# Optimization experiments

Hardware: AMD Instinct MI355X
Metric: run time of the kernel (lower is better)

## Reference

```python
import jax, jax.numpy as jnp
import numpy as np

D_MODEL = 1024
N_HEADS = 16
HEAD_DIM = D_MODEL // N_HEADS


def setup_inputs() -> dict:
    key = jax.random.key(0)
    ks = jax.random.split(key, 5)
    T, B = 2048, 2
    x = jax.random.normal(ks[0], (T, B, D_MODEL), dtype=jnp.float32)
    s = 1.0 / np.sqrt(D_MODEL)
    Wq = jax.random.normal(ks[1], (D_MODEL, D_MODEL), dtype=jnp.float32) * s
    Wk = jax.random.normal(ks[2], (D_MODEL, D_MODEL), dtype=jnp.float32) * s
    Wv = jax.random.normal(ks[3], (D_MODEL, D_MODEL), dtype=jnp.float32) * s
    Wo = jax.random.normal(ks[4], (D_MODEL, D_MODEL), dtype=jnp.float32) * s
    return {"x": x, "Wq": Wq, "Wk": Wk, "Wv": Wv, "Wo": Wo}


def reference(x, Wq, Wk, Wv, Wo):
    T, B, C = x.shape
    H, D = N_HEADS, HEAD_DIM

    def split_heads(t):
        # (T,B,C) -> (B,H,T,D), matching view+permute(1,2,0,3)
        return t.reshape(T, B, H, D).transpose(1, 2, 0, 3)

    q = split_heads(x @ Wq.T)
    k = split_heads(x @ Wk.T)
    v = split_heads(x @ Wv.T)

    scale = 1.0 / jnp.sqrt(jnp.asarray(D, dtype=x.dtype))
    scores = jnp.einsum('bhqd,bhkd->bhqk', q, k) * scale  # (B,H,T,T)
    causal = jnp.tril(jnp.ones((T, T), dtype=bool))
    scores = jnp.where(causal, scores, jnp.asarray(-jnp.inf, dtype=scores.dtype))
    probs = jax.nn.softmax(scores, axis=-1)
    ctx = jnp.einsum('bhqk,bhkd->bhqd', probs, v)  # (B,H,T,D)
    ctx = ctx.transpose(2, 0, 1, 3).reshape(T, B, C)
    return ctx @ Wo.T
```

## Files before the change

### kernel.cpp

```cpp
#include <hip/hip_runtime.h>
#include <hip/hip_bf16.h>

#define TT 2048
#define BB 2
#define CC 1024
#define HH 16
#define DD 64
#define MM (TT * BB)

typedef short bf16x8 __attribute__((ext_vector_type(8)));
typedef float f32x4  __attribute__((ext_vector_type(4)));

__device__ inline ushort f2b(float f) {
    union { float f; unsigned u; } v; v.f = f;
    unsigned r = v.u + 0x7FFFu + ((v.u >> 16) & 1u);
    return (ushort)(r >> 16);
}

__device__ inline unsigned pack_bf16(float a, float b) {
    __hip_bfloat162 h = __float22bfloat162_rn(make_float2(a, b));
    union { __hip_bfloat162 h; unsigned u; } c; c.h = h;
    return c.u;
}

__device__ inline void gload_lds16(const ushort* g, ushort* l) {
    __builtin_amdgcn_global_load_lds(
        (const __attribute__((address_space(1))) void*)g,
        (__attribute__((address_space(3))) void*)l, 16, 0, 0);
}

#define XQUADS (MM * CC / 4)
#define WQUADS (CC * CC / 4)
__global__ __launch_bounds__(256) void conv_all(const float* __restrict__ x,
                                                const float* __restrict__ Wq,
                                                const float* __restrict__ Wk,
                                                const float* __restrict__ Wv,
                                                const float* __restrict__ Wo,
                                                ushort* __restrict__ dst) {
    int idx = blockIdx.x * 256 + threadIdx.x;
    const float* src;
    int off;
    if (idx < XQUADS) {
        src = x; off = idx;
    } else {
        int wi = (idx - XQUADS) >> 18;
        off = (idx - XQUADS) & (WQUADS - 1);
        src = (wi == 0) ? Wq : (wi == 1) ? Wk : (wi == 2) ? Wv : Wo;
    }
    float4 v = ((const float4*)src)[off];
    ushort4 o = {f2b(v.x), f2b(v.y), f2b(v.z), f2b(v.w)};
    ((ushort4*)dst)[idx] = o;
}

__global__ __launch_bounds__(256) void gemm_qkv(const ushort* __restrict__ A,
                                                const ushort* __restrict__ B0,
                                                const ushort* __restrict__ B1,
                                                const ushort* __restrict__ B2,
                                                ushort* __restrict__ Oq,
                                                ushort* __restrict__ Ok,
                                                ushort* __restrict__ Ov) {
    __shared__ __align__(16) ushort As[128 * 32];
    __shared__ __align__(16) ushort Bs[128 * 32];

    const int tid = threadIdx.x;
    const int wave = tid >> 6, lane = tid & 63;
    const int quad = lane >> 4, l16 = lane & 15;
    const int wm = wave >> 1, wn = wave & 1;

    const int bm = blockIdx.x * 128;
    const int by = blockIdx.y;
    const int wsel = by >> 3;
    const ushort* Bp = (wsel == 0) ? B0 : (wsel == 1) ? B1 : B2;
    const int bn = (by & 7) * 128;

    const int srow = lane >> 2;
    const int scol = (lane & 3) * 8;

    f32x4 acc[4][4];
#pragma unroll
    for (int i = 0; i < 4; i++)
#pragma unroll
        for (int j = 0; j < 4; j++) acc[i][j] = (f32x4){0.f, 0.f, 0.f, 0.f};

    for (int k0 = 0; k0 < CC; k0 += 32) {
#pragma unroll
        for (int i = 0; i < 2; i++) {
            const int rbase = wave * 32 + i * 16;
            gload_lds16(A + (size_t)(bm + rbase + srow) * CC + k0 + scol,
                        As + rbase * 32);
            gload_lds16(Bp + (size_t)(bn + rbase + srow) * CC + k0 + scol,
                        Bs + rbase * 32);
        }
        __syncthreads();

        bf16x8 af[4], bf[4];
#pragma unroll
        for (int mi = 0; mi < 4; mi++)
            af[mi] = *(const bf16x8*)(As + (wm * 64 + mi * 16 + l16) * 32 + quad * 8);
#pragma unroll
        for (int ni = 0; ni < 4; ni++)
            bf[ni] = *(const bf16x8*)(Bs + (wn * 64 + ni * 16 + l16) * 32 + quad * 8);
#pragma unroll
        for (int mi = 0; mi < 4; mi++)
#pragma unroll
            for (int ni = 0; ni < 4; ni++)
                acc[mi][ni] = __builtin_amdgcn_mfma_f32_16x16x32_bf16(
                    af[mi], bf[ni], acc[mi][ni], 0, 0, 0);
        __syncthreads();
    }

#pragma unroll
    for (int mi = 0; mi < 4; mi++) {
#pragma unroll
        for (int r = 0; r < 4; r++) {
            const int m = bm + wm * 64 + mi * 16 + quad * 4 + r;
#pragma unroll
            for (int ni = 0; ni < 4; ni++) {
                const int colg = bn + wn * 64 + ni * 16 + l16;
                float v = acc[mi][ni][r];
                if (wsel == 0) v *= 0.18033688f;
                const int t = m >> 1, b = m & 1;
                const int h = colg >> 6, d = colg & 63;
                ushort* dst = (wsel == 0) ? Oq : (wsel == 1) ? Ok : Ov;
                dst[(((size_t)(b * HH + h)) * TT + t) * DD + d] = f2b(v);
            }
        }
    }
}

__global__ __launch_bounds__(256) void gemm_out(const ushort* __restrict__ A,
                                                const ushort* __restrict__ Bm,
                                                float* __restrict__ Of) {
    __shared__ __align__(16) ushort As[128 * 32];
    __shared__ __align__(16) ushort Bs[64 * 32];

    const int tid = threadIdx.x;
    const int wave = tid >> 6, lane = tid & 63;
    const int quad = lane >> 4, l16 = lane & 15;

    const int bm = blockIdx.x * 128;
    const int bn = blockIdx.y * 64;

    const int srow = lane >> 2;
    const int scol = (lane & 3) * 8;

    f32x4 acc[2][4];
#pragma unroll
    for (int i = 0; i < 2; i++)
#pragma unroll
        for (int j = 0; j < 4; j++) acc[i][j] = (f32x4){0.f, 0.f, 0.f, 0.f};

    for (int k0 = 0; k0 < CC; k0 += 32) {
#pragma unroll
        for (int i = 0; i < 2; i++) {
            const int rbase = wave * 32 + i * 16;
            gload_lds16(A + (size_t)(bm + rbase + srow) * CC + k0 + scol,
                        As + rbase * 32);
        }
        gload_lds16(Bm + (size_t)(bn + wave * 16 + srow) * CC + k0 + scol,
                    Bs + wave * 16 * 32);
        __syncthreads();

        bf16x8 af[2], bf[4];
#pragma unroll
        for (int mi = 0; mi < 2; mi++)
            af[mi] = *(const bf16x8*)(As + (wave * 32 + mi * 16 + l16) * 32 + quad * 8);
#pragma unroll
        for (int ni = 0; ni < 4; ni++)
            bf[ni] = *(const bf16x8*)(Bs + (ni * 16 + l16) * 32 + quad * 8);
#pragma unroll
        for (int mi = 0; mi < 2; mi++)
#pragma unroll
            for (int ni = 0; ni < 4; ni++)
                acc[mi][ni] = __builtin_amdgcn_mfma_f32_16x16x32_bf16(
                    af[mi], bf[ni], acc[mi][ni], 0, 0, 0);
        __syncthreads();
    }

#pragma unroll
    for (int mi = 0; mi < 2; mi++)
#pragma unroll
        for (int r = 0; r < 4; r++) {
            const int m = bm + wave * 32 + mi * 16 + quad * 4 + r;
#pragma unroll
            for (int ni = 0; ni < 4; ni++)
                Of[(size_t)m * CC + bn + ni * 16 + l16] = acc[mi][ni][r];
        }
}

__global__ __launch_bounds__(256) void prep_kv(const ushort* __restrict__ Kb,
                                               const ushort* __restrict__ Vb,
                                               ushort* __restrict__ Kf,
                                               ushort* __restrict__ Vf) {
    __shared__ __align__(16) ushort Ls[64 * 72];
    const int tile = blockIdx.x;
    const int bh   = blockIdx.y;
    const int t    = threadIdx.x;
    const size_t src = (size_t)bh * TT * DD + (size_t)tile * 64 * DD;
    const size_t dst = (size_t)bh * TT * DD + (size_t)tile * 4096;

#pragma unroll
    for (int i = 0; i < 2; i++) {
        int e = t + i * 256;
        int r = e >> 3, kc = (e & 7) * 8;
        *(uint4*)(Ls + r * 72 + kc) = *(const uint4*)(Kb + src + r * 64 + kc);
    }
    __syncthreads();
#pragma unroll
    for (int i = 0; i < 2; i++) {
        int o = t + i * 256;
        int c = o >> 8, nb = (o >> 6) & 3, lane = o & 63;
        int quad = lane >> 4, l16 = lane & 15;
        int j = nb * 16 + l16, k0 = c * 32 + quad * 8;
        *(uint4*)(Kf + dst + (size_t)o * 8) = *(const uint4*)(Ls + j * 72 + k0);
    }
    __syncthreads();

#pragma unroll
    for (int i = 0; i < 2; i++) {
        int e = t + i * 256;
        int r = e >> 3, kc = (e & 7) * 8;
        *(uint4*)(Ls + r * 72 + kc) = *(const uint4*)(Vb + src + r * 64 + kc);
    }
    __syncthreads();
#pragma unroll
    for (int i = 0; i < 2; i++) {
        int o = t + i * 256;
        int c = o >> 8, db = (o >> 6) & 3, lane = o & 63;
        int quad = lane >> 4, l16 = lane & 15;
        int d = db * 16 + l16;
        ushort tmp[8];
#pragma unroll
        for (int u = 0; u < 8; u++) {
            int j = 16 * ((8 * c + u) >> 2) + 4 * quad + (u & 3);
            tmp[u] = Ls[j * 72 + d];
        }
        *(uint4*)(Vf + dst + (size_t)o * 8) = *(uint4*)tmp;
    }
}

template <bool DIAG>
__device__ __forceinline__ void attn_step64(const bf16x8* qa,
                                            f32x4* O,
                                            float* l,
                                            const bf16x8* kf, const bf16x8* vf,
                                            int j0, int qg0, int quad) {
#pragma unroll
    for (int m = 0; m < 2; m++) {
        f32x4 S[4];
#pragma unroll
        for (int nb = 0; nb < 4; nb++) S[nb] = (f32x4){0.f, 0.f, 0.f, 0.f};
#pragma unroll
        for (int c = 0; c < 2; c++)
#pragma unroll
            for (int nb = 0; nb < 4; nb++)
                S[nb] = __builtin_amdgcn_mfma_f32_16x16x32_bf16(
                    kf[c * 4 + nb], qa[m * 2 + c], S[nb], 0, 0, 0);

        const int qg = qg0 + m * 16;
        float p[4][4];
#pragma unroll
        for (int nb = 0; nb < 4; nb++)
#pragma unroll
            for (int r = 0; r < 4; r++) {
                float s = S[nb][r];
                if (DIAG) { if (j0 + nb * 16 + quad * 4 + r > qg) s = -1e30f; }
                p[nb][r] = __builtin_amdgcn_exp2f(s);
            }
#pragma unroll
        for (int nb = 0; nb < 4; nb++)
            l[m] += (p[nb][0] + p[nb][1]) + (p[nb][2] + p[nb][3]);

        union { unsigned w[4]; bf16x8 v; } pa0, pa1;
#pragma unroll
        for (int w = 0; w < 4; w++) {
            const int nb = w >> 1;
            const int rb = (w & 1) * 2;
            pa0.w[w] = pack_bf16(p[nb][rb], p[nb][rb + 1]);
            pa1.w[w] = pack_bf16(p[2 + nb][rb], p[2 + nb][rb + 1]);
        }
#pragma unroll
        for (int db = 0; db < 4; db++)
            O[m * 4 + db] = __builtin_amdgcn_mfma_f32_16x16x32_bf16(
                pa0.v, vf[db], O[m * 4 + db], 0, 0, 0);
#pragma unroll
        for (int db = 0; db < 4; db++)
            O[m * 4 + db] = __builtin_amdgcn_mfma_f32_16x16x32_bf16(
                pa1.v, vf[4 + db], O[m * 4 + db], 0, 0, 0);
    }
}

__global__ __launch_bounds__(256, 1) void attn_mfma(const ushort* __restrict__ Qb,
                                                    const ushort* __restrict__ Kf,
                                                    const ushort* __restrict__ Vf,
                                                    ushort* __restrict__ ctx) {
    __shared__ __align__(16) ushort KV[2][8192];

    const int tid  = threadIdx.x;
    const int wave = tid >> 6;
    const int lane = tid & 63;
    const int quad = lane >> 4;
    const int l16  = lane & 15;

    const int bidx = blockIdx.x;
    const int xcd  = bidx & 7;
    const int slot = bidx >> 3;
    const int bh   = xcd * 4 + (slot >> 3);
    const int p    = slot & 7;

    const int qtA = p, qtB = 15 - p;
    const int q0A = qtA * 128 + wave * 32;
    const int q0B = qtB * 128 + wave * 32;
    const int qgA = q0A + l16;
    const int qgB = q0B + l16;

    const size_t baseQK = (size_t)bh * TT * DD;

    bf16x8 qaA[4], qaB[4];
#pragma unroll
    for (int m = 0; m < 2; m++) {
        const ushort* qp = Qb + baseQK + (size_t)(q0A + m * 16 + l16) * DD + quad * 8;
        qaA[m * 2 + 0] = *(const bf16x8*)(qp);
        qaA[m * 2 + 1] = *(const bf16x8*)(qp + 32);
        const ushort* qp2 = Qb + baseQK + (size_t)(q0B + m * 16 + l16) * DD + quad * 8;
        qaB[m * 2 + 0] = *(const bf16x8*)(qp2);
        qaB[m * 2 + 1] = *(const bf16x8*)(qp2 + 32);
    }

    f32x4 OA[8], OB[8];
#pragma unroll
    for (int i = 0; i < 8; i++) {
        OA[i] = (f32x4){0.f, 0.f, 0.f, 0.f};
        OB[i] = (f32x4){0.f, 0.f, 0.f, 0.f};
    }
    float lA[2] = {0.f, 0.f}, lB[2] = {0.f, 0.f};

    const int dA = 2 * qtA + (wave >> 1);
    const int dB = 2 * qtB + (wave >> 1);
    const int ktmax = 2 * qtB + 1;

    const ushort* Kfp = Kf + baseQK;
    const ushort* Vfp = Vf + baseQK;

    auto stage = [&](int buf, const ushort* kp, const ushort* vp) {
#pragma unroll
        for (int i = 0; i < 2; i++) {
            const int ch = wave * 2 + i;
            gload_lds16(kp + (ch << 9) + lane * 8, &KV[buf][ch << 9]);
            gload_lds16(vp + (ch << 9) + lane * 8, &KV[buf][(8 + ch) << 9]);
        }
    };

    stage(0, Kfp, Vfp);
    __syncthreads();

    int cur = 0;
    for (int kt = 0; kt <= ktmax; kt++) {
        if (kt < ktmax) stage(cur ^ 1, Kfp + 4096, Vfp + 4096);

        bf16x8 kf[8], vf[8];
#pragma unroll
        for (int i = 0; i < 8; i++) {
            kf[i] = *(const bf16x8*)(&KV[cur][i << 9] + lane * 8);
            vf[i] = *(const bf16x8*)(&KV[cur][(8 + i) << 9] + lane * 8);
        }

        const int j0 = kt * 64;
        if (kt < dB)
            attn_step64<false>(qaB, OB, lB, kf, vf, j0, qgB, quad);
        else if (kt == dB)
            attn_step64<true >(qaB, OB, lB, kf, vf, j0, qgB, quad);

        if (kt < dA)
            attn_step64<false>(qaA, OA, lA, kf, vf, j0, qgA, quad);
        else if (kt == dA)
            attn_step64<true >(qaA, OA, lA, kf, vf, j0, qgA, quad);

        __syncthreads();
        cur ^= 1;
        Kfp += 4096;
        Vfp += 4096;
    }

#pragma unroll
    for (int m = 0; m < 2; m++) {
        lA[m] += __shfl_xor(lA[m], 16); lA[m] += __shfl_xor(lA[m], 32);
        lB[m] += __shfl_xor(lB[m], 16); lB[m] += __shfl_xor(lB[m], 32);
    }

    const int b = bh >> 4, h = bh & 15;
#pragma unroll
    for (int m = 0; m < 2; m++)
#pragma unroll
        for (int r = 0; r < 4; r++) {
            const float invA = 1.f / __shfl(lA[m], quad * 4 + r);
            const float invB = 1.f / __shfl(lB[m], quad * 4 + r);
            const int tA = q0A + m * 16 + quad * 4 + r;
            const int tB = q0B + m * 16 + quad * 4 + r;
#pragma unroll
            for (int db = 0; db < 4; db++) {
                ctx[((size_t)tA * BB + b) * CC + h * DD + db * 16 + l16] =
                    f2b(OA[m * 4 + db][r] * invA);
                ctx[((size_t)tB * BB + b) * CC + h * DD + db * 16 + l16] =
                    f2b(OB[m * 4 + db][r] * invB);
            }
        }
}

extern "C" void kernel_launch(void* const* d_in, const int* in_sizes, int n_in,
                              void* d_out, int out_size, void* d_ws, size_t ws_size,
                              hipStream_t stream) {
    const float* x  = (const float*)d_in[0];
    const float* Wq = (const float*)d_in[1];
    const float* Wk = (const float*)d_in[2];
    const float* Wv = (const float*)d_in[3];
    const float* Wo = (const float*)d_in[4];
    float* out = (float*)d_out;

    ushort* xb  = (ushort*)d_ws;
    ushort* Wb  = xb + (size_t)MM * CC;
    ushort* Wqb = Wb;
    ushort* Wkb = Wb + (size_t)CC * CC;
    ushort* Wvb = Wb + 2 * (size_t)CC * CC;
    ushort* Wob = Wb + 3 * (size_t)CC * CC;
    ushort* Qb  = Wb + 4 * (size_t)CC * CC;
    ushort* Kb  = Qb + (size_t)MM * CC;
    ushort* Vb  = Kb + (size_t)MM * CC;
    ushort* Kf  = Vb + (size_t)MM * CC;
    ushort* Vf  = Kf + (size_t)MM * CC;
    ushort* Ctxb = Vf + (size_t)MM * CC;

    conv_all<<<dim3((XQUADS + 4 * WQUADS) / 256), 256, 0, stream>>>(
        x, Wq, Wk, Wv, Wo, xb);

    gemm_qkv<<<dim3(MM / 128, 24), 256, 0, stream>>>(
        xb, Wqb, Wkb, Wvb, Qb, Kb, Vb);

    prep_kv<<<dim3(TT / 64, BB * HH), 256, 0, stream>>>(Kb, Vb, Kf, Vf);

    attn_mfma<<<dim3(256), 256, 0, stream>>>(Qb, Kf, Vf, Ctxb);

    gemm_out<<<dim3(MM / 128, CC / 64), 256, 0, stream>>>(Ctxb, Wob, out);
}
```

Measured before the change: 178.1 us.

## Split attention key tiles across wave pairs and double block count

Each attention block now covers 64 query rows per tile pair instead of 128. The four waves are arranged as two query halves times two key halves, and each wave processes 32 keys per 64-key tile. Partial O and row sums from the second key-half wave are reduced through shared memory before normalization and store. The grid doubles to 512 blocks and launch bounds allow 2 blocks per CU, which should improve occupancy and load balance. The cost is an extra LDS reduction and sync at the end, plus redundant Q loads per block.

```diff
diff --git a/kernel.cpp b/kernel.cpp
--- a/kernel.cpp
+++ b/kernel.cpp
@@ -240,79 +240,77 @@
 }
 
 template <bool DIAG>
-__device__ __forceinline__ void attn_step64(const bf16x8* qa,
-                                            f32x4* O,
-                                            float* l,
-                                            const bf16x8* kf, const bf16x8* vf,
-                                            int j0, int qg0, int quad) {
+__device__ __forceinline__ void attn_step(const bf16x8* qa,
+                                          f32x4* O,
+                                          float* l,
+                                          const bf16x8* kfr,
+                                          const bf16x8* vfr,
+                                          int key0, int qg0, int quad) {
 #pragma unroll
     for (int m = 0; m < 2; m++) {
-        f32x4 S[4];
-#pragma unroll
-        for (int nb = 0; nb < 4; nb++) S[nb] = (f32x4){0.f, 0.f, 0.f, 0.f};
+        f32x4 S[2];
+        S[0] = (f32x4){0.f, 0.f, 0.f, 0.f};
+        S[1] = (f32x4){0.f, 0.f, 0.f, 0.f};
 #pragma unroll
         for (int c = 0; c < 2; c++)
 #pragma unroll
-            for (int nb = 0; nb < 4; nb++)
-                S[nb] = __builtin_amdgcn_mfma_f32_16x16x32_bf16(
-                    kf[c * 4 + nb], qa[m * 2 + c], S[nb], 0, 0, 0);
+            for (int nbl = 0; nbl < 2; nbl++)
+                S[nbl] = __builtin_amdgcn_mfma_f32_16x16x32_bf16(
+                    kfr[c * 2 + nbl], qa[m * 2 + c], S[nbl], 0, 0, 0);
 
         const int qg = qg0 + m * 16;
-        float p[4][4];
-#pragma unroll
-        for (int nb = 0; nb < 4; nb++)
+        float p[2][4];
+#pragma unroll
+        for (int nbl = 0; nbl < 2; nbl++)
 #pragma unroll
             for (int r = 0; r < 4; r++) {
-                float s = S[nb][r];
-                if (DIAG) { if (j0 + nb * 16 + quad * 4 + r > qg) s = -1e30f; }
-                p[nb][r] = __builtin_amdgcn_exp2f(s);
+                float s = S[nbl][r];
+                if (DIAG) { if (key0 + nbl * 16 + quad * 4 + r > qg) s = -1e30f; }
+                p[nbl][r] = __builtin_amdgcn_exp2f(s);
             }
-#pragma unroll
-        for (int nb = 0; nb < 4; nb++)
-            l[m] += (p[nb][0] + p[nb][1]) + (p[nb][2] + p[nb][3]);
-
-        union { unsigned w[4]; bf16x8 v; } pa0, pa1;
-#pragma unroll
-        for (int w = 0; w < 4; w++) {
-            const int nb = w >> 1;
-            const int rb = (w & 1) * 2;
-            pa0.w[w] = pack_bf16(p[nb][rb], p[nb][rb + 1]);
-            pa1.w[w] = pack_bf16(p[2 + nb][rb], p[2 + nb][rb + 1]);
-        }
+        l[m] += (p[0][0] + p[0][1] + p[0][2] + p[0][3]) +
+                (p[1][0] + p[1][1] + p[1][2] + p[1][3]);
+
+        union { unsigned w[4]; bf16x8 v; } pa;
+#pragma unroll
+        for (int w = 0; w < 4; w++)
+            pa.w[w] = pack_bf16(p[w >> 1][(w & 1) * 2],
+                                p[w >> 1][(w & 1) * 2 + 1]);
 #pragma unroll
         for (int db = 0; db < 4; db++)
             O[m * 4 + db] = __builtin_amdgcn_mfma_f32_16x16x32_bf16(
-                pa0.v, vf[db], O[m * 4 + db], 0, 0, 0);
-#pragma unroll
-        for (int db = 0; db < 4; db++)
-            O[m * 4 + db] = __builtin_amdgcn_mfma_f32_16x16x32_bf16(
-                pa1.v, vf[4 + db], O[m * 4 + db], 0, 0, 0);
-    }
-}
-
-__global__ __launch_bounds__(256, 1) void attn_mfma(const ushort* __restrict__ Qb,
+                pa.v, vfr[db], O[m * 4 + db], 0, 0, 0);
+    }
+}
+
+__global__ __launch_bounds__(256, 2) void attn_mfma(const ushort* __restrict__ Qb,
                                                     const ushort* __restrict__ Kf,
                                                     const ushort* __restrict__ Vf,
                                                     ushort* __restrict__ ctx) {
     __shared__ __align__(16) ushort KV[2][8192];
+    __shared__ float Lsum[2][2][2][64];
 
     const int tid  = threadIdx.x;
     const int wave = tid >> 6;
     const int lane = tid & 63;
     const int quad = lane >> 4;
     const int l16  = lane & 15;
+    const int kh   = wave & 1;
+    const int qh   = wave >> 1;
 
     const int bidx = blockIdx.x;
     const int xcd  = bidx & 7;
     const int slot = bidx >> 3;
-    const int bh   = xcd * 4 + (slot >> 3);
-    const int p    = slot & 7;
-
-    const int qtA = p, qtB = 15 - p;
-    const int q0A = qtA * 128 + wave * 32;
-    const int q0B = qtB * 128 + wave * 32;
+    const int bh   = xcd * 4 + (slot >> 4);
+    const int p    = slot & 15;
+
+    const int qtA = p, qtB = (TT / 64 - 1) - p;
+    const int q0A = qtA * 64 + qh * 32;
+    const int q0B = qtB * 64 + qh * 32;
     const int qgA = q0A + l16;
     const int qgB = q0B + l16;
+    const int qidxA = 2 * qtA + qh;
+    const int qidxB = 2 * qtB + qh;
 
     const size_t baseQK = (size_t)bh * TT * DD;
 
@@ -335,10 +333,6 @@
     }
     float lA[2] = {0.f, 0.f}, lB[2] = {0.f, 0.f};
 
-    const int dA = 2 * qtA + (wave >> 1);
-    const int dB = 2 * qtB + (wave >> 1);
-    const int ktmax = 2 * qtB + 1;
-
     const ushort* Kfp = Kf + baseQK;
     const ushort* Vfp = Vf + baseQK;
 
@@ -355,26 +349,32 @@
     __syncthreads();
 
     int cur = 0;
-    for (int kt = 0; kt <= ktmax; kt++) {
-        if (kt < ktmax) stage(cur ^ 1, Kfp + 4096, Vfp + 4096);
-
-        bf16x8 kf[8], vf[8];
-#pragma unroll
-        for (int i = 0; i < 8; i++) {
-            kf[i] = *(const bf16x8*)(&KV[cur][i << 9] + lane * 8);
-            vf[i] = *(const bf16x8*)(&KV[cur][(8 + i) << 9] + lane * 8);
-        }
-
-        const int j0 = kt * 64;
-        if (kt < dB)
-            attn_step64<false>(qaB, OB, lB, kf, vf, j0, qgB, quad);
-        else if (kt == dB)
-            attn_step64<true >(qaB, OB, lB, kf, vf, j0, qgB, quad);
-
-        if (kt < dA)
-            attn_step64<false>(qaA, OA, lA, kf, vf, j0, qgA, quad);
-        else if (kt == dA)
-            attn_step64<true >(qaA, OA, lA, kf, vf, j0, qgA, quad);
+    for (int kt = 0; kt <= qtB; kt++) {
+        if (kt < qtB) stage(cur ^ 1, Kfp + 4096, Vfp + 4096);
+
+        bf16x8 kfr[4], vfr[4];
+#pragma unroll
+        for (int c = 0; c < 2; c++)
+#pragma unroll
+            for (int nbl = 0; nbl < 2; nbl++)
+                kfr[c * 2 + nbl] =
+                    *(const bf16x8*)(&KV[cur][(c * 4 + 2 * kh + nbl) << 9] + lane * 8);
+#pragma unroll
+        for (int db = 0; db < 4; db++)
+            vfr[db] = *(const bf16x8*)(&KV[cur][(8 + kh * 4 + db) << 9] + lane * 8);
+
+        const int sidx = 2 * kt + kh;
+        const int key0 = kt * 64 + kh * 32;
+
+        if (sidx < qidxB)
+            attn_step<false>(qaB, OB, lB, kfr, vfr, key0, qgB, quad);
+        else if (sidx == qidxB)
+            attn_step<true >(qaB, OB, lB, kfr, vfr, key0, qgB, quad);
+
+        if (sidx < qidxA)
+            attn_step<false>(qaA, OA, lA, kfr, vfr, key0, qgA, quad);
+        else if (sidx == qidxA)
+            attn_step<true >(qaA, OA, lA, kfr, vfr, key0, qgA, quad);
 
         __syncthreads();
         cur ^= 1;
@@ -388,23 +388,52 @@
         lB[m] += __shfl_xor(lB[m], 16); lB[m] += __shfl_xor(lB[m], 32);
     }
 
-    const int b = bh >> 4, h = bh & 15;
-#pragma unroll
-    for (int m = 0; m < 2; m++)
-#pragma unroll
-        for (int r = 0; r < 4; r++) {
-            const float invA = 1.f / __shfl(lA[m], quad * 4 + r);
-            const float invB = 1.f / __shfl(lB[m], quad * 4 + r);
-            const int tA = q0A + m * 16 + quad * 4 + r;
-            const int tB = q0B + m * 16 + quad * 4 + r;
-#pragma unroll
-            for (int db = 0; db < 4; db++) {
-                ctx[((size_t)tA * BB + b) * CC + h * DD + db * 16 + l16] =
-                    f2b(OA[m * 4 + db][r] * invA);
-                ctx[((size_t)tB * BB + b) * CC + h * DD + db * 16 + l16] =
-                    f2b(OB[m * 4 + db][r] * invB);
+    float* scr = (float*)&KV[0][0];
+    if (kh == 1) {
+#pragma unroll
+        for (int i = 0; i < 8; i++) {
+            const int idx = qh * 4096 + i * 256 + lane * 4;
+            *(f32x4*)&scr[idx]        = OA[i];
+            *(f32x4*)&scr[idx + 2048] = OB[i];
+        }
+#pragma unroll
+        for (int m = 0; m < 2; m++) {
+            Lsum[qh][0][m][lane] = lA[m];
+            Lsum[qh][1][m][lane] = lB[m];
+        }
+    }
+    __syncthreads();
+    if (kh == 0) {
+#pragma unroll
+        for (int i = 0; i < 8; i++) {
+            const int idx = qh * 4096 + i * 256 + lane * 4;
+            OA[i] += *(const f32x4*)&scr[idx];
+            OB[i] += *(const f32x4*)&scr[idx + 2048];
+        }
+#pragma unroll
+        for (int m = 0; m < 2; m++) {
+            lA[m] += Lsum[qh][0][m][lane];
+            lB[m] += Lsum[qh][1][m][lane];
+        }
+
+        const int bb = bh >> 4, hd = bh & 15;
+#pragma unroll
+        for (int m = 0; m < 2; m++)
+#pragma unroll
+            for (int r = 0; r < 4; r++) {
+                const float invA = 1.f / __shfl(lA[m], quad * 4 + r);
+                const float invB = 1.f / __shfl(lB[m], quad * 4 + r);
+                const int tA = q0A + m * 16 + quad * 4 + r;
+                const int tB = q0B + m * 16 + quad * 4 + r;
+#pragma unroll
+                for (int db = 0; db < 4; db++) {
+                    ctx[((size_t)tA * BB + bb) * CC + hd * DD + db * 16 + l16] =
+                        f2b(OA[m * 4 + db][r] * invA);
+                    ctx[((size_t)tB * BB + bb) * CC + hd * DD + db * 16 + l16] =
+                        f2b(OB[m * 4 + db][r] * invB);
+                }
             }
-        }
+    }
 }
 
 extern "C" void kernel_launch(void* const* d_in, const int* in_sizes, int n_in,
@@ -438,7 +467,7 @@
 
     prep_kv<<<dim3(TT / 64, BB * HH), 256, 0, stream>>>(Kb, Vb, Kf, Vf);
 
-    attn_mfma<<<dim3(256), 256, 0, stream>>>(Qb, Kf, Vf, Ctxb);
+    attn_mfma<<<dim3(512), 256, 0, stream>>>(Qb, Kf, Vf, Ctxb);
 
     gemm_out<<<dim3(MM / 128, CC / 64), 256, 0, stream>>>(Ctxb, Wob, out);
 }
```

Result: faster. 173.1 us (-2.8%).
